# Optimization experiments

Hardware: AMD Instinct MI355X
Metric: run time of the kernel (lower is better)

## Reference

```python
import jax, jax.numpy as jnp
import numpy as np

B, T, C, H = 4, 2048, 1024, 16
D = C // H  # head dim = 64


def _layernorm(x, g, b, eps=1e-5):
    mu = jnp.mean(x, axis=-1, keepdims=True)
    var = jnp.var(x, axis=-1, keepdims=True)
    return (x - mu) * jax.lax.rsqrt(var + eps) * g + b


def setup_inputs() -> dict:
    key = jax.random.key(0)
    ks = jax.random.split(key, 8)
    s = 0.02
    return {
        "x": jax.random.normal(ks[0], (B, T, C), dtype=jnp.float32),
        "ln1_g": jnp.ones((C,), jnp.float32),
        "ln1_b": jnp.zeros((C,), jnp.float32),
        "W_qkv": jax.random.normal(ks[1], (C, 3 * C), dtype=jnp.float32) * s,
        "b_qkv": jnp.zeros((3 * C,), jnp.float32),
        "W_o": jax.random.normal(ks[2], (C, C), dtype=jnp.float32) * s,
        "b_o": jnp.zeros((C,), jnp.float32),
        "ln2_g": jnp.ones((C,), jnp.float32),
        "ln2_b": jnp.zeros((C,), jnp.float32),
        "W_fc": jax.random.normal(ks[3], (C, 4 * C), dtype=jnp.float32) * s,
        "b_fc": jnp.zeros((4 * C,), jnp.float32),
        "W_pr": jax.random.normal(ks[4], (4 * C, C), dtype=jnp.float32) * s,
        "b_pr": jnp.zeros((C,), jnp.float32),
    }


def reference(x, ln1_g, ln1_b, W_qkv, b_qkv, W_o, b_o, ln2_g, ln2_b, W_fc, b_fc, W_pr, b_pr):
    # --- attention sub-block ---
    h = _layernorm(x, ln1_g, ln1_b)
    qkv = h @ W_qkv + b_qkv                       # [B,T,3C]
    q, k, v = jnp.split(qkv, 3, axis=-1)
    q = q.reshape(B, T, H, D).transpose(0, 2, 1, 3)  # [B,H,T,D]
    k = k.reshape(B, T, H, D).transpose(0, 2, 1, 3)
    v = v.reshape(B, T, H, D).transpose(0, 2, 1, 3)
    att = jnp.einsum("bhqd,bhkd->bhqk", q, k) * (1.0 / jnp.sqrt(jnp.float32(D)))
    causal = jnp.tril(jnp.ones((T, T), dtype=bool))
    att = jnp.where(causal, att, jnp.float32(-jnp.inf))
    att = jax.nn.softmax(att, axis=-1)
    y = jnp.einsum("bhqk,bhkd->bhqd", att, v)     # [B,H,T,D]
    y = y.transpose(0, 2, 1, 3).reshape(B, T, C)
    y = y @ W_o + b_o
    x = x + y
    # --- FFN sub-block ---
    h2 = _layernorm(x, ln2_g, ln2_b)
    f = jax.nn.gelu(h2 @ W_fc + b_fc, approximate=False)  # nn.GELU default = exact
    f = f @ W_pr + b_pr
    return x + f
```

## Files before the change

### kernel.cpp

```cpp
#include <hip/hip_runtime.h>
#include <math.h>
#include <stdint.h>

#define Bz 4
#define Tz 2048
#define Cz 1024
#define Hz 16
#define Dz 64
#define MTOK (Bz*Tz)

typedef __attribute__((ext_vector_type(8))) short short8;
typedef __attribute__((ext_vector_type(4))) short short4v;
typedef __attribute__((ext_vector_type(4))) float f32x4;

typedef unsigned int u32_g __attribute__((address_space(1)));
typedef unsigned int u32_l __attribute__((address_space(3)));

__device__ __forceinline__ unsigned short f2bf(float f) {
    unsigned int u = __float_as_uint(f);
    u += 0x7fffu + ((u >> 16) & 1u);
    return (unsigned short)(u >> 16);
}
__device__ __forceinline__ float bf2f(unsigned short h) {
    return __uint_as_float((unsigned int)h << 16);
}

__device__ __forceinline__ void async_cp16(const unsigned short* g, unsigned short* l) {
    __builtin_amdgcn_global_load_lds((const u32_g*)g, (u32_l*)l, 16, 0, 0);
}

#define BARX() asm volatile("s_barrier" ::: "memory")
#define VMCM(n) asm volatile("s_waitcnt vmcnt(" #n ")" ::: "memory")

__global__ void transpose_wf(const float* __restrict__ W, unsigned short* __restrict__ Bf,
                             int K, int N) {
    const int nf = blockIdx.x;
    const int k0 = blockIdx.y * 128;
    const int tid = threadIdx.x;
    const int ktl = tid >> 6, lane = tid & 63;
    const int col = nf * 16 + (lane & 15);
    const int kk = k0 + ktl * 32 + (lane >> 4) * 8;
    const int KT = K >> 5;
    short8 o;
    #pragma unroll
    for (int j = 0; j < 8; j++)
        o[j] = (short)f2bf(W[(size_t)(kk + j) * N + col]);
    *(short8*)&Bf[(((size_t)nf * KT + (k0 >> 5) + ktl) * 64 + lane) * 8] = o;
}

__global__ void transpose_v(const unsigned short* __restrict__ in, unsigned short* __restrict__ out) {
    __shared__ unsigned short tile[64][68];
    const int bh = blockIdx.x;
    const int t0 = blockIdx.y * 64;
    const int tid = threadIdx.x;
    const int r4 = tid >> 4;
    const int c4 = tid & 15;
    #pragma unroll
    for (int p = 0; p < 4; p++) {
        const int r = p * 16 + r4;
        *(short4v*)&tile[r][c4 * 4] =
            *(const short4v*)&in[((size_t)bh * Tz + t0 + r) * Dz + c4 * 4];
    }
    __syncthreads();
    #pragma unroll
    for (int p = 0; p < 4; p++) {
        const int d = p * 16 + r4;
        short4v o;
        #pragma unroll
        for (int j = 0; j < 4; j++) o[j] = tile[c4 * 4 + j][d];
        *(short4v*)&out[((size_t)bh * Dz + d) * Tz + t0 + c4 * 4] = o;
    }
}

__global__ void ln_kernel(const float* __restrict__ x, const float* __restrict__ g,
                          const float* __restrict__ bb, unsigned short* __restrict__ out) {
    int tok = blockIdx.x, tid = threadIdx.x;
    const float4 v = ((const float4*)(x + (size_t)tok * Cz))[tid];
    float s = v.x + v.y + v.z + v.w;
    float sq = v.x * v.x + v.y * v.y + v.z * v.z + v.w * v.w;
    #pragma unroll
    for (int m = 1; m < 64; m <<= 1) { s += __shfl_xor(s, m); sq += __shfl_xor(sq, m); }
    __shared__ float red[8];
    int lane = tid & 63, wid = tid >> 6;
    if (!lane) { red[wid] = s; red[4 + wid] = sq; }
    __syncthreads();
    s = red[0] + red[1] + red[2] + red[3];
    sq = red[4] + red[5] + red[6] + red[7];
    float mu = s * (1.0f / Cz);
    float var = sq * (1.0f / Cz) - mu * mu;
    float rs = rsqrtf(var + 1e-5f);
    float4 gv = ((const float4*)g)[tid];
    float4 bv = ((const float4*)bb)[tid];
    short4v o;
    o[0] = f2bf((v.x - mu) * rs * gv.x + bv.x);
    o[1] = f2bf((v.y - mu) * rs * gv.y + bv.y);
    o[2] = f2bf((v.z - mu) * rs * gv.z + bv.z);
    o[3] = f2bf((v.w - mu) * rs * gv.w + bv.w);
    *(short4v*)(out + (size_t)tok * Cz + tid * 4) = o;
}

#define MODE_QKV 0
#define MODE_RESID 1
#define MODE_GELU 2

template <int MODE, int WM>
__launch_bounds__(512, 1)
__global__ void gemm_bg(const unsigned short* __restrict__ A, const unsigned short* __restrict__ Bf,
                        int K, int N, const float* __restrict__ bias,
                        float* __restrict__ outf, unsigned short* __restrict__ outb,
                        const float* __restrict__ resid,
                        unsigned short* __restrict__ qo, unsigned short* __restrict__ ko,
                        unsigned short* __restrict__ vo) {
    constexpr int MI = WM / 16;
    constexpr int BM = 2 * WM;
    constexpr int SLOT = BM * 32;
    constexpr int AC = BM / 128;
    constexpr int MT = 8192 / BM;
    constexpr int MT8 = MT / 8;
    __shared__ __align__(16) unsigned short LDS[4 * SLOT];

    const int tid = threadIdx.x;
    const int lane = tid & 63;
    const int wid = tid >> 6;
    const int quad = lane >> 4, l15 = lane & 15;
    const int gm = wid >> 2, gn = wid & 3;
    const int id = blockIdx.x;
    const int rr = id >> 3;
    const int m0 = ((id & 7) * MT8 + (rr % MT8)) * BM;
    const int n0 = (rr / MT8) * 256;
    const int NT = K >> 5;
    const int KT = K >> 5;

    const int lseg = (tid & 3) ^ ((tid >> 3) & 3);
    const int srow = tid >> 2;
    const unsigned short* Ag0 = A + (size_t)(m0 + srow) * K + lseg * 8;
    const unsigned short* Ag1 = A + (size_t)(m0 + 128 + srow) * K + lseg * 8;

    int offA[MI];
    #pragma unroll
    for (int mi = 0; mi < MI; mi++) {
        const int ra = gm * WM + mi * 16 + l15;
        offA[mi] = ra * 32 + ((quad ^ ((ra >> 1) & 3)) << 3);
    }

    const int nfg = (n0 >> 4) + gn * 4;
    const unsigned short* Bp[4];
    #pragma unroll
    for (int ni = 0; ni < 4; ni++)
        Bp[ni] = Bf + ((size_t)(nfg + ni) * KT) * 512 + lane * 8;

    f32x4 acc[MI][4] = {};
    short8 af[MI], bfP[4], bfQ[4];

#define GLB(bfX) do { _Pragma("unroll") for (int ni = 0; ni < 4; ni++) { \
    asm volatile("global_load_dwordx4 %0, %1, off" \
        : "=&v"(bfX[ni]) : "v"((unsigned long long)(uintptr_t)Bp[ni]) : "memory"); \
    Bp[ni] += 512; } } while (0)
#define STG(tt) do { unsigned short* sp_ = LDS + (((unsigned)(tt)) & 3u) * SLOT; \
    const size_t kof_ = (size_t)(tt) * 32; \
    async_cp16(Ag0 + kof_, sp_ + tid * 8); \
    if constexpr (AC == 2) async_cp16(Ag1 + kof_, sp_ + 4096 + tid * 8); } while (0)
#define RDS(tt) do { const unsigned short* sp_ = LDS + (((unsigned)(tt)) & 3u) * SLOT; \
    _Pragma("unroll") for (int mi = 0; mi < MI; mi++) af[mi] = *(const short8*)(sp_ + offA[mi]); } while (0)
#define MMS(bfX) do { \
    __builtin_amdgcn_s_setprio(1); \
    _Pragma("unroll") for (int mi = 0; mi < MI; mi++) \
        _Pragma("unroll") for (int ni = 0; ni < 4; ni++) \
            acc[mi][ni] = __builtin_amdgcn_mfma_f32_16x16x32_bf16(af[mi], bfX[ni], acc[mi][ni], 0, 0, 0); \
    __builtin_amdgcn_s_setprio(0); } while (0)
#define WAITV(tt) do { \
    if ((tt) == 0)            { if constexpr (AC == 2) VMCM(4); else VMCM(2); } \
    else if ((tt) >= NT - 2)  { VMCM(0); } \
    else                      { if constexpr (AC == 2) VMCM(2); else VMCM(1); } } while (0)

    GLB(bfP);
    STG(0); STG(1); STG(2);

    for (int t = 0; t < NT; t += 2) {
        WAITV(t);
        BARX();
        if (t + 1 < NT) GLB(bfQ);
        if (t + 3 < NT) STG(t + 3);
        RDS(t);
        MMS(bfP);
        WAITV(t + 1);
        BARX();
        if (t + 2 < NT) GLB(bfP);
        if (t + 4 < NT) STG(t + 4);
        RDS(t + 1);
        MMS(bfQ);
    }
#undef GLB
#undef STG
#undef RDS
#undef MMS
#undef WAITV

    float bv[4];
    #pragma unroll
    for (int ni = 0; ni < 4; ni++) bv[ni] = bias[n0 + gn * 64 + ni * 16 + l15];

    if constexpr (MODE == MODE_QKV) {
        const int colb = n0 + gn * 64;
        const int which = colb >> 10;
        const int hh = (colb & 1023) >> 6;
        unsigned short* dst = (which == 0) ? qo : (which == 1) ? ko : vo;
        #pragma unroll
        for (int mi = 0; mi < MI; mi++) {
            #pragma unroll
            for (int r = 0; r < 4; r++) {
                const int row = m0 + gm * WM + mi * 16 + quad * 4 + r;
                const int b_ = row >> 11, tt = row & 2047;
                unsigned short* rp = dst + ((size_t)(b_ * Hz + hh) * Tz + tt) * Dz;
                #pragma unroll
                for (int ni = 0; ni < 4; ni++)
                    rp[ni * 16 + l15] = f2bf(acc[mi][ni][r] + bv[ni]);
            }
        }
    } else if constexpr (MODE == MODE_RESID) {
        #pragma unroll
        for (int mi = 0; mi < MI; mi++) {
            #pragma unroll
            for (int r = 0; r < 4; r++) {
                const int row = m0 + gm * WM + mi * 16 + quad * 4 + r;
                float* rp = outf + (size_t)row * N + n0 + gn * 64;
                const float* rr_ = resid + (size_t)row * N + n0 + gn * 64;
                #pragma unroll
                for (int ni = 0; ni < 4; ni++) {
                    const int c = ni * 16 + l15;
                    rp[c] = acc[mi][ni][r] + bv[ni] + rr_[c];
                }
            }
        }
    } else {
        #pragma unroll
        for (int mi = 0; mi < MI; mi++) {
            #pragma unroll
            for (int r = 0; r < 4; r++) {
                const int row = m0 + gm * WM + mi * 16 + quad * 4 + r;
                unsigned short* rp = outb + (size_t)row * N + n0 + gn * 64;
                #pragma unroll
                for (int ni = 0; ni < 4; ni++) {
                    float val = acc[mi][ni][r] + bv[ni];
                    float c = val * (1.0f + 0.044715f * val * val);
                    float e = __expf(1.5957691216057308f * c);
                    rp[ni * 16 + l15] = f2bf(val * e / (1.0f + e));
                }
            }
        }
    }
}

#define ATT_SC 0.18033688011112042f
__launch_bounds__(256)
__global__ void attn_kernel(const unsigned short* __restrict__ qb, const unsigned short* __restrict__ kb,
                            const unsigned short* __restrict__ vt, unsigned short* __restrict__ y) {
    __shared__ __align__(16) unsigned short Klds[64 * 64];
    __shared__ __align__(16) unsigned short Vtl[64 * 64];
    __shared__ __align__(16) unsigned short Plds[4][16 * 72];
    const int tid = threadIdx.x;
    const int lane = tid & 63, wid = tid >> 6;
    const int quad = lane >> 4, l15 = lane & 15;
    const int bh = blockIdx.x & 63;
    const int qt = 15 - (int)(blockIdx.x >> 6);
    const size_t baseT = (size_t)bh * Tz;
    const size_t vbase = (size_t)bh * Dz;
    const int qb0 = qt * 128;

    short8 qf[2][2];
    {
        const unsigned short* q0p = qb + (baseT + qb0 + wid * 16 + l15) * Dz + quad * 8;
        qf[0][0] = *(const short8*)q0p;
        qf[0][1] = *(const short8*)(q0p + 32);
        const unsigned short* q1p = q0p + (size_t)64 * Dz;
        qf[1][0] = *(const short8*)q1p;
        qf[1][1] = *(const short8*)(q1p + 32);
    }

    f32x4 o[2][4] = {};
    float lsum[2][4] = {{0.f,0.f,0.f,0.f},{0.f,0.f,0.f,0.f}};

    const int srow = lane >> 3;
    const int swz = ((lane & 7) ^ srow) * 8;
    const unsigned short* kg0 = kb + (baseT + wid * 8 + srow) * Dz + swz;
    const unsigned short* kg1 = kg0 + (size_t)32 * Dz;
    const unsigned short* vg0 = vt + (vbase + wid * 8 + srow) * Tz + swz;
    const unsigned short* vg1 = vg0 + (size_t)32 * Tz;
    unsigned short* kl0 = &Klds[wid * 512 + lane * 8];
    unsigned short* kl1 = kl0 + 2048;
    unsigned short* vl0 = &Vtl[wid * 512 + lane * 8];
    unsigned short* vl1 = vl0 + 2048;

    const int nchunk = 2 * qt + 2;

    for (int ci = 0; ci < nchunk; ci++) {
        const int k0 = ci * 64;
        async_cp16(kg0 + (size_t)k0 * Dz, kl0);
        async_cp16(kg1 + (size_t)k0 * Dz, kl1);
        async_cp16(vg0 + k0, vl0);
        async_cp16(vg1 + k0, vl1);
        __syncthreads();

        #pragma unroll
        for (int t = 0; t < 2; t++) {
            if (t == 0 && ci == nchunk - 1) continue;
            const bool diag = (ci == nchunk - 2 + t);

            f32x4 s[4];
            #pragma unroll
            for (int c = 0; c < 4; c++) {
                const int rk = c * 16 + l15;
                short8 kf0 = *(const short8*)&Klds[rk * 64 + ((quad ^ (rk & 7)) * 8)];
                short8 kf1 = *(const short8*)&Klds[rk * 64 + (((quad + 4) ^ (rk & 7)) * 8)];
                f32x4 z = {};
                z = __builtin_amdgcn_mfma_f32_16x16x32_bf16(qf[t][0], kf0, z, 0, 0, 0);
                s[c] = __builtin_amdgcn_mfma_f32_16x16x32_bf16(qf[t][1], kf1, z, 0, 0, 0);
            }
            const int qr = qb0 + t * 64 + wid * 16 + quad * 4;
            #pragma unroll
            for (int c = 0; c < 4; c++)
                #pragma unroll
                for (int r = 0; r < 4; r++) {
                    float p = exp2f(s[c][r] * ATT_SC);
                    if (diag) {
                        int key = k0 + c * 16 + l15;
                        p = (key <= qr + r) ? p : 0.f;
                    }
                    s[c][r] = p;
                    lsum[t][r] += p;
                }
            unsigned short* P = Plds[wid];
            #pragma unroll
            for (int c = 0; c < 4; c++)
                #pragma unroll
                for (int r = 0; r < 4; r++)
                    P[(quad * 4 + r) * 72 + c * 16 + l15] = f2bf(s[c][r]);
            short8 pf0 = *(const short8*)&P[l15 * 72 + quad * 8];
            short8 pf1 = *(const short8*)&P[l15 * 72 + 32 + quad * 8];
            #pragma unroll
            for (int nc = 0; nc < 4; nc++) {
                const int rv = nc * 16 + l15;
                short8 vf0 = *(const short8*)&Vtl[rv * 64 + ((quad ^ (rv & 7)) * 8)];
                short8 vf1 = *(const short8*)&Vtl[rv * 64 + (((quad + 4) ^ (rv & 7)) * 8)];
                o[t][nc] = __builtin_amdgcn_mfma_f32_16x16x32_bf16(pf0, vf0, o[t][nc], 0, 0, 0);
                o[t][nc] = __builtin_amdgcn_mfma_f32_16x16x32_bf16(pf1, vf1, o[t][nc], 0, 0, 0);
            }
        }
        __syncthreads();
    }

    const int b_ = bh >> 4, hh = bh & 15;
    #pragma unroll
    for (int t = 0; t < 2; t++)
        #pragma unroll
        for (int r = 0; r < 4; r++) {
            float ls = lsum[t][r];
            #pragma unroll
            for (int m = 1; m < 16; m <<= 1) ls += __shfl_xor(ls, m);
            float inv = 1.0f / ls;
            size_t tok = (size_t)qb0 + t * 64 + wid * 16 + quad * 4 + r;
            unsigned short* yr = y + ((size_t)b_ * Tz + tok) * Cz + hh * Dz;
            #pragma unroll
            for (int nc = 0; nc < 4; nc++)
                yr[nc * 16 + l15] = f2bf(o[t][nc][r] * inv);
        }
}

extern "C" void kernel_launch(void* const* d_in, const int* in_sizes, int n_in,
                              void* d_out, int out_size, void* d_ws, size_t ws_size,
                              hipStream_t stream) {
    const float* x    = (const float*)d_in[0];
    const float* ln1g = (const float*)d_in[1];
    const float* ln1b = (const float*)d_in[2];
    const float* Wqkv = (const float*)d_in[3];
    const float* bqkv = (const float*)d_in[4];
    const float* Wo   = (const float*)d_in[5];
    const float* bo   = (const float*)d_in[6];
    const float* ln2g = (const float*)d_in[7];
    const float* ln2b = (const float*)d_in[8];
    const float* Wfc  = (const float*)d_in[9];
    const float* bfc  = (const float*)d_in[10];
    const float* Wpr  = (const float*)d_in[11];
    const float* bpr  = (const float*)d_in[12];
    float* out = (float*)d_out;

    char* ws = (char*)d_ws;
    size_t off = 0;
    auto alloc = [&](size_t bytes) { void* p = ws + off; off += (bytes + 255) & ~(size_t)255; return p; };
    unsigned short* wqkv_t = (unsigned short*)alloc((size_t)3072 * 1024 * 2);
    unsigned short* wo_t   = (unsigned short*)alloc((size_t)1024 * 1024 * 2);
    unsigned short* wfc_t  = (unsigned short*)alloc((size_t)4096 * 1024 * 2);
    unsigned short* wpr_t  = (unsigned short*)alloc((size_t)1024 * 4096 * 2);
    unsigned short* h1     = (unsigned short*)alloc((size_t)MTOK * Cz * 2);
    unsigned short* qbuf   = (unsigned short*)alloc((size_t)MTOK * Cz * 2);
    unsigned short* kbuf   = (unsigned short*)alloc((size_t)MTOK * Cz * 2);
    unsigned short* vbuf   = (unsigned short*)alloc((size_t)MTOK * Cz * 2);
    unsigned short* ybuf   = (unsigned short*)alloc((size_t)MTOK * Cz * 2);
    float*          x1     = (float*)alloc((size_t)MTOK * Cz * 4);
    unsigned short* h2     = (unsigned short*)alloc((size_t)MTOK * Cz * 2);
    unsigned short* fbuf   = (unsigned short*)alloc((size_t)MTOK * 4096 * 2);
    unsigned short* vtmp   = fbuf;

    transpose_wf<<<dim3(3072 / 16, 1024 / 128), 256, 0, stream>>>(Wqkv, wqkv_t, 1024, 3072);
    transpose_wf<<<dim3(1024 / 16, 1024 / 128), 256, 0, stream>>>(Wo, wo_t, 1024, 1024);
    transpose_wf<<<dim3(4096 / 16, 1024 / 128), 256, 0, stream>>>(Wfc, wfc_t, 1024, 4096);
    transpose_wf<<<dim3(1024 / 16, 4096 / 128), 256, 0, stream>>>(Wpr, wpr_t, 4096, 1024);

    ln_kernel<<<MTOK, 256, 0, stream>>>(x, ln1g, ln1b, h1);
    gemm_bg<MODE_QKV, 64><<<768, 512, 0, stream>>>(h1, wqkv_t, 1024, 3072, bqkv,
                                                   nullptr, nullptr, nullptr, qbuf, kbuf, vtmp);
    transpose_v<<<dim3(64, 32), 256, 0, stream>>>(vtmp, vbuf);
    attn_kernel<<<1024, 256, 0, stream>>>(qbuf, kbuf, vbuf, ybuf);
    gemm_bg<MODE_RESID, 64><<<256, 512, 0, stream>>>(ybuf, wo_t, 1024, 1024, bo,
                                                     x1, nullptr, x, nullptr, nullptr, nullptr);
    ln_kernel<<<MTOK, 256, 0, stream>>>(x1, ln2g, ln2b, h2);
    gemm_bg<MODE_GELU, 128><<<512, 512, 0, stream>>>(h2, wfc_t, 1024, 4096, bfc,
                                                     nullptr, fbuf, nullptr, nullptr, nullptr, nullptr);
    gemm_bg<MODE_RESID, 64><<<256, 512, 0, stream>>>(fbuf, wpr_t, 4096, 1024, bpr,
                                                     out, nullptr, x1, nullptr, nullptr, nullptr);
}
```

Before: 516.1 us.

## Replace GEMM with 64x256-tile 256-thread kernel and register-prefetched LDS pipeline

Replaces the 512-thread templated GEMM, which used 128/256-row tiles, with a fixed 64x256 tile kernel of 4 waves. It double-buffers both A fragments (read from LDS via inline ds_read_b128) and B fragments (global loads into registers), using explicit lgkmcnt/vmcnt waits so LDS reads for the next k-step overlap the current MFMAs. The smaller tile doubles or quadruples grid size for better occupancy and load balance. In exchange each B fragment is reused across fewer rows, so more global traffic goes to weights.

```diff
diff --git a/kernel.cpp b/kernel.cpp
--- a/kernel.cpp
+++ b/kernel.cpp
@@ -31,6 +31,8 @@
 
 #define BARX() asm volatile("s_barrier" ::: "memory")
 #define VMCM(n) asm volatile("s_waitcnt vmcnt(" #n ")" ::: "memory")
+#define LGKMC(n) do { asm volatile("s_waitcnt lgkmcnt(" #n ")" ::: "memory"); \
+                      __builtin_amdgcn_sched_barrier(0); } while (0)
 
 __global__ void transpose_wf(const float* __restrict__ W, unsigned short* __restrict__ Bf,
                              int K, int N) {
@@ -103,44 +105,36 @@
 #define MODE_RESID 1
 #define MODE_GELU 2
 
-template <int MODE, int WM>
-__launch_bounds__(512, 1)
-__global__ void gemm_bg(const unsigned short* __restrict__ A, const unsigned short* __restrict__ Bf,
+template <int MODE>
+__launch_bounds__(256)
+__global__ void gemm_rp(const unsigned short* __restrict__ A, const unsigned short* __restrict__ Bf,
                         int K, int N, const float* __restrict__ bias,
                         float* __restrict__ outf, unsigned short* __restrict__ outb,
                         const float* __restrict__ resid,
                         unsigned short* __restrict__ qo, unsigned short* __restrict__ ko,
                         unsigned short* __restrict__ vo) {
-    constexpr int MI = WM / 16;
-    constexpr int BM = 2 * WM;
-    constexpr int SLOT = BM * 32;
-    constexpr int AC = BM / 128;
-    constexpr int MT = 8192 / BM;
-    constexpr int MT8 = MT / 8;
-    __shared__ __align__(16) unsigned short LDS[4 * SLOT];
-
+    __shared__ __align__(16) unsigned short LDS[4 * 2048];
     const int tid = threadIdx.x;
     const int lane = tid & 63;
-    const int wid = tid >> 6;
+    const int gn = tid >> 6;
     const int quad = lane >> 4, l15 = lane & 15;
-    const int gm = wid >> 2, gn = wid & 3;
     const int id = blockIdx.x;
     const int rr = id >> 3;
-    const int m0 = ((id & 7) * MT8 + (rr % MT8)) * BM;
-    const int n0 = (rr / MT8) * 256;
+    const int m0 = ((id & 7) * 16 + (rr & 15)) * 64;
+    const int n0 = (rr >> 4) * 256;
     const int NT = K >> 5;
     const int KT = K >> 5;
 
     const int lseg = (tid & 3) ^ ((tid >> 3) & 3);
     const int srow = tid >> 2;
     const unsigned short* Ag0 = A + (size_t)(m0 + srow) * K + lseg * 8;
-    const unsigned short* Ag1 = A + (size_t)(m0 + 128 + srow) * K + lseg * 8;
-
-    int offA[MI];
-    #pragma unroll
-    for (int mi = 0; mi < MI; mi++) {
-        const int ra = gm * WM + mi * 16 + l15;
-        offA[mi] = ra * 32 + ((quad ^ ((ra >> 1) & 3)) << 3);
+
+    const unsigned ldsA = (unsigned)(uintptr_t)(u32_l*)LDS;
+    unsigned offAb[4];
+    #pragma unroll
+    for (int mi = 0; mi < 4; mi++) {
+        const int ra = mi * 16 + l15;
+        offAb[mi] = (unsigned)(ra * 64 + ((quad ^ ((ra >> 1) & 3)) << 4));
     }
 
     const int nfg = (n0 >> 4) + gn * 4;
@@ -149,52 +143,49 @@
     for (int ni = 0; ni < 4; ni++)
         Bp[ni] = Bf + ((size_t)(nfg + ni) * KT) * 512 + lane * 8;
 
-    f32x4 acc[MI][4] = {};
-    short8 af[MI], bfP[4], bfQ[4];
-
-#define GLB(bfX) do { _Pragma("unroll") for (int ni = 0; ni < 4; ni++) { \
+    f32x4 acc[4][4] = {};
+    short8 afP[4], afQ[4], bfP[4], bfQ[4];
+
+#define GLBa(bfX) do { _Pragma("unroll") for (int ni = 0; ni < 4; ni++) { \
     asm volatile("global_load_dwordx4 %0, %1, off" \
         : "=&v"(bfX[ni]) : "v"((unsigned long long)(uintptr_t)Bp[ni]) : "memory"); \
     Bp[ni] += 512; } } while (0)
-#define STG(tt) do { unsigned short* sp_ = LDS + (((unsigned)(tt)) & 3u) * SLOT; \
-    const size_t kof_ = (size_t)(tt) * 32; \
-    async_cp16(Ag0 + kof_, sp_ + tid * 8); \
-    if constexpr (AC == 2) async_cp16(Ag1 + kof_, sp_ + 4096 + tid * 8); } while (0)
-#define RDS(tt) do { const unsigned short* sp_ = LDS + (((unsigned)(tt)) & 3u) * SLOT; \
-    _Pragma("unroll") for (int mi = 0; mi < MI; mi++) af[mi] = *(const short8*)(sp_ + offA[mi]); } while (0)
-#define MMS(bfX) do { \
+#define STG(tt) async_cp16(Ag0 + (size_t)(tt) * 32, LDS + (((unsigned)(tt)) & 3u) * 2048 + tid * 8)
+#define RDSa(afX, tt) do { \
+    const unsigned sb_ = ldsA + (((unsigned)(tt)) & 3u) * 4096u; \
+    _Pragma("unroll") for (int mi = 0; mi < 4; mi++) \
+        asm volatile("ds_read_b128 %0, %1" : "=&v"(afX[mi]) : "v"(sb_ + offAb[mi])); } while (0)
+#define MMS(afX, bfX) do { \
     __builtin_amdgcn_s_setprio(1); \
-    _Pragma("unroll") for (int mi = 0; mi < MI; mi++) \
+    _Pragma("unroll") for (int mi = 0; mi < 4; mi++) \
         _Pragma("unroll") for (int ni = 0; ni < 4; ni++) \
-            acc[mi][ni] = __builtin_amdgcn_mfma_f32_16x16x32_bf16(af[mi], bfX[ni], acc[mi][ni], 0, 0, 0); \
+            acc[mi][ni] = __builtin_amdgcn_mfma_f32_16x16x32_bf16(afX[mi], bfX[ni], acc[mi][ni], 0, 0, 0); \
     __builtin_amdgcn_s_setprio(0); } while (0)
-#define WAITV(tt) do { \
-    if ((tt) == 0)            { if constexpr (AC == 2) VMCM(4); else VMCM(2); } \
-    else if ((tt) >= NT - 2)  { VMCM(0); } \
-    else                      { if constexpr (AC == 2) VMCM(2); else VMCM(1); } } while (0)
-
-    GLB(bfP);
-    STG(0); STG(1); STG(2);
+
+    STG(0); STG(1); GLBa(bfP); GLBa(bfQ); STG(2);
+    VMCM(5);
+    BARX();
+    RDSa(afP, 0);
 
     for (int t = 0; t < NT; t += 2) {
-        WAITV(t);
+        if (t + 3 < NT) STG(t + 3);
+        RDSa(afQ, t + 1);
+        LGKMC(4);
+        MMS(afP, bfP);
+        if (t + 2 < NT) GLBa(bfP);
+        if (t + 3 < NT) { VMCM(5); } else { VMCM(0); }
         BARX();
-        if (t + 1 < NT) GLB(bfQ);
-        if (t + 3 < NT) STG(t + 3);
-        RDS(t);
-        MMS(bfP);
-        WAITV(t + 1);
+        if (t + 4 < NT) STG(t + 4);
+        if (t + 2 < NT) { RDSa(afP, t + 2); LGKMC(4); } else { LGKMC(0); }
+        MMS(afQ, bfQ);
+        if (t + 3 < NT) GLBa(bfQ);
+        if (t + 4 < NT) { VMCM(5); } else { VMCM(0); }
         BARX();
-        if (t + 2 < NT) GLB(bfP);
-        if (t + 4 < NT) STG(t + 4);
-        RDS(t + 1);
-        MMS(bfQ);
-    }
-#undef GLB
+    }
+#undef GLBa
 #undef STG
-#undef RDS
+#undef RDSa
 #undef MMS
-#undef WAITV
 
     float bv[4];
     #pragma unroll
@@ -206,10 +197,10 @@
         const int hh = (colb & 1023) >> 6;
         unsigned short* dst = (which == 0) ? qo : (which == 1) ? ko : vo;
         #pragma unroll
-        for (int mi = 0; mi < MI; mi++) {
+        for (int mi = 0; mi < 4; mi++) {
             #pragma unroll
             for (int r = 0; r < 4; r++) {
-                const int row = m0 + gm * WM + mi * 16 + quad * 4 + r;
+                const int row = m0 + mi * 16 + quad * 4 + r;
                 const int b_ = row >> 11, tt = row & 2047;
                 unsigned short* rp = dst + ((size_t)(b_ * Hz + hh) * Tz + tt) * Dz;
                 #pragma unroll
@@ -219,10 +210,10 @@
         }
     } else if constexpr (MODE == MODE_RESID) {
         #pragma unroll
-        for (int mi = 0; mi < MI; mi++) {
+        for (int mi = 0; mi < 4; mi++) {
             #pragma unroll
             for (int r = 0; r < 4; r++) {
-                const int row = m0 + gm * WM + mi * 16 + quad * 4 + r;
+                const int row = m0 + mi * 16 + quad * 4 + r;
                 float* rp = outf + (size_t)row * N + n0 + gn * 64;
                 const float* rr_ = resid + (size_t)row * N + n0 + gn * 64;
                 #pragma unroll
@@ -234,10 +225,10 @@
         }
     } else {
         #pragma unroll
-        for (int mi = 0; mi < MI; mi++) {
+        for (int mi = 0; mi < 4; mi++) {
             #pragma unroll
             for (int r = 0; r < 4; r++) {
-                const int row = m0 + gm * WM + mi * 16 + quad * 4 + r;
+                const int row = m0 + mi * 16 + quad * 4 + r;
                 unsigned short* rp = outb + (size_t)row * N + n0 + gn * 64;
                 #pragma unroll
                 for (int ni = 0; ni < 4; ni++) {
@@ -407,15 +398,15 @@
     transpose_wf<<<dim3(1024 / 16, 4096 / 128), 256, 0, stream>>>(Wpr, wpr_t, 4096, 1024);
 
     ln_kernel<<<MTOK, 256, 0, stream>>>(x, ln1g, ln1b, h1);
-    gemm_bg<MODE_QKV, 64><<<768, 512, 0, stream>>>(h1, wqkv_t, 1024, 3072, bqkv,
-                                                   nullptr, nullptr, nullptr, qbuf, kbuf, vtmp);
+    gemm_rp<MODE_QKV><<<1536, 256, 0, stream>>>(h1, wqkv_t, 1024, 3072, bqkv,
+                                                nullptr, nullptr, nullptr, qbuf, kbuf, vtmp);
     transpose_v<<<dim3(64, 32), 256, 0, stream>>>(vtmp, vbuf);
     attn_kernel<<<1024, 256, 0, stream>>>(qbuf, kbuf, vbuf, ybuf);
-    gemm_bg<MODE_RESID, 64><<<256, 512, 0, stream>>>(ybuf, wo_t, 1024, 1024, bo,
-                                                     x1, nullptr, x, nullptr, nullptr, nullptr);
+    gemm_rp<MODE_RESID><<<512, 256, 0, stream>>>(ybuf, wo_t, 1024, 1024, bo,
+                                                 x1, nullptr, x, nullptr, nullptr, nullptr);
     ln_kernel<<<MTOK, 256, 0, stream>>>(x1, ln2g, ln2b, h2);
-    gemm_bg<MODE_GELU, 128><<<512, 512, 0, stream>>>(h2, wfc_t, 1024, 4096, bfc,
-                                                     nullptr, fbuf, nullptr, nullptr, nullptr, nullptr);
-    gemm_bg<MODE_RESID, 64><<<256, 512, 0, stream>>>(fbuf, wpr_t, 4096, 1024, bpr,
-                                                     out, nullptr, x1, nullptr, nullptr, nullptr);
-}
+    gemm_rp<MODE_GELU><<<2048, 256, 0, stream>>>(h2, wfc_t, 1024, 4096, bfc,
+                                                 nullptr, fbuf, nullptr, nullptr, nullptr, nullptr);
+    gemm_rp<MODE_RESID><<<512, 256, 0, stream>>>(fbuf, wpr_t, 4096, 1024, bpr,
+                                                 out, nullptr, x1, nullptr, nullptr, nullptr);
+}
```

Measured after the change: 499.8 us. 1.03x faster.
